# Kernel optimization log

Hardware: AMD Instinct MI355X
Metric: run time of the kernel (lower is better)

Reference implementation:

```python
import math
import jax, jax.numpy as jnp
import numpy as np

N_NODES = 10000
N_EDGES = 160000
N_BASIS = 10
MAX_RADIUS = 5.0
NUM_NEIGHBORS = 16.0
LMAX = 2
MUL_IN = 8
MULS = (32, 16, 10)  # mul[l] = max(4, 32 // (l+1))

# ---------- real Clebsch-Gordan (Wigner) coupling tensors ----------

def _cg_complex(j1, m1, j2, m2, j3, m3):
    if m1 + m2 != m3:
        return 0.0
    f = math.factorial
    pref = math.sqrt((2 * j3 + 1) * f(j1 + j2 - j3) * f(j1 - j2 + j3) * f(-j1 + j2 + j3) / f(j1 + j2 + j3 + 1))
    pref *= math.sqrt(f(j1 + m1) * f(j1 - m1) * f(j2 + m2) * f(j2 - m2) * f(j3 + m3) * f(j3 - m3))
    s = 0.0
    for k in range(max(0, j2 - j3 - m1, j1 - j3 + m2), min(j1 + j2 - j3, j1 - m1, j2 + m2) + 1):
        s += (-1.0) ** k / (f(k) * f(j1 + j2 - j3 - k) * f(j1 - m1 - k) * f(j2 + m2 - k) * f(j3 - j2 + m1 + k) * f(j3 - j1 - m2 + k))
    return pref * s

def _q_matrix(l):
    # complex -> real spherical-harmonic change of basis, rows/cols ordered m = -l..l
    Q = np.zeros((2 * l + 1, 2 * l + 1), dtype=np.complex128)
    Q[l, l] = 1.0
    s2 = 1.0 / math.sqrt(2.0)
    for m in range(1, l + 1):
        Q[l + m, l + m] = (-1) ** m * s2
        Q[l + m, l - m] = s2
        Q[l - m, l - m] = 1j * s2
        Q[l - m, l + m] = -1j * (-1) ** m * s2
    return Q

def _real_cg(l1, l2, l3):
    C = np.zeros((2 * l1 + 1, 2 * l2 + 1, 2 * l3 + 1), dtype=np.complex128)
    for m1 in range(-l1, l1 + 1):
        for m2 in range(-l2, l2 + 1):
            m3 = m1 + m2
            if abs(m3) <= l3:
                C[l1 + m1, l2 + m2, l3 + m3] = _cg_complex(l1, m1, l2, m2, l3, m3)
    K = np.einsum('ia,jb,kc,abc->ijk', _q_matrix(l1).conj(), _q_matrix(l2).conj(), _q_matrix(l3), C)
    K = (1j * K).real if np.abs(K.imag).max() > np.abs(K.real).max() else K.real
    K = K / np.linalg.norm(K) * math.sqrt(2 * l3 + 1)  # component-style path normalization
    return K.astype(np.float32)

PATHS_IN = [(0, 0, 0), (0, 1, 1), (0, 2, 2)]
PATHS_HID = [(li, lf, lo) for li in range(LMAX + 1) for lf in range(LMAX + 1)
             for lo in range(LMAX + 1) if abs(li - lf) <= lo <= li + lf]
PATHS_OUT = [(0, 0, 0), (1, 1, 0), (2, 2, 0)]
CG = {(l1, l2, l3): jnp.asarray(_real_cg(l1, l2, l3))
      for l1 in range(LMAX + 1) for l2 in range(LMAX + 1) for l3 in range(LMAX + 1)
      if abs(l1 - l2) <= l3 <= l1 + l2}

# ---------- edge features ----------

def spherical_harmonics(vec):
    # component-normalized real SH l=0..2 of the normalized edge vector, m = -l..l
    n = vec / jnp.linalg.norm(vec, axis=-1, keepdims=True)
    x, y, z = n[:, 0], n[:, 1], n[:, 2]
    c3, c15, c5 = math.sqrt(3.0), math.sqrt(15.0), math.sqrt(5.0)
    y0 = jnp.ones_like(x)[:, None]
    y1 = c3 * jnp.stack([y, z, x], -1)
    y2 = jnp.stack([c15 * x * y, c15 * y * z, 0.5 * c5 * (3.0 * z * z - 1.0),
                    c15 * x * z, 0.5 * c15 * (x * x - y * y)], -1)
    return {0: y0, 1: y1, 2: y2}

def radial_embedding(r):
    # soft_one_hot_linspace(..., basis='smooth_finite', cutoff=True) * sqrt(n_basis)
    centers = jnp.linspace(0.0, MAX_RADIUS, N_BASIS + 2)[1:-1]
    step = MAX_RADIUS / (N_BASIS + 1)
    d = (r[:, None] - centers) / step
    u = lambda t: jnp.where(t > 0.0, jnp.exp(-1.0 / jnp.where(t > 0.0, t, 1.0)), 0.0)
    return (1.14136 * math.e ** 2 * math.sqrt(N_BASIS)) * u(d + 1.0) * u(1.0 - d)

# ---------- equivariant convolution (gather -> CG tensor product -> scatter) ----------

def conv(feats, edge_src, edge_dst, Y, emb, fw1, fw2, paths, lin):
    n_nodes = feats[0].shape[0]
    w = jax.nn.silu(emb @ fw1) @ fw2            # [E, sum of mul_in over paths]
    by_lo = {0: [], 1: [], 2: []}
    off = 0
    for li, lf, lo in paths:
        f = feats[li][edge_src]                  # gather  [E, mul, 2li+1]
        mul = f.shape[1]
        pw = w[:, off:off + mul]                 # per-edge 'uvu' path weights
        off += mul
        msg = jnp.einsum('eui,ej,ijk,eu->euk', f, Y[lf], CG[(li, lf, lo)], pw)
        by_lo[lo].append(jax.ops.segment_sum(msg, edge_dst, num_segments=n_nodes))
    out = {}
    inv = 1.0 / math.sqrt(NUM_NEIGHBORS)
    for lo, parts in by_lo.items():
        if parts:
            out[lo] = jnp.einsum('nui,uv->nvi', jnp.concatenate(parts, axis=1) * inv, lin[lo])
    return out

def gate(feats, gw):
    s = feats[0][:, :, 0]
    g = jax.nn.sigmoid(s @ gw)                   # [N, mul1 + mul2] gate scalars
    m1 = feats[1].shape[1]
    return {0: jax.nn.silu(feats[0]),
            1: feats[1] * g[:, :m1, None],
            2: feats[2] * g[:, m1:, None]}

# ---------- inputs ----------

def setup_inputs() -> dict:
    ks = iter(jax.random.split(jax.random.key(0), 32))
    def init(shape, fan_in):
        return jax.random.normal(next(ks), shape, jnp.float32) / math.sqrt(fan_in)
    m0, m1, m2 = MULS
    return {
        'x': jax.random.normal(next(ks), (N_NODES, MUL_IN), jnp.float32),
        'edge_vec': 1.2 * jax.random.normal(next(ks), (N_EDGES, 3), jnp.float32),
        'fc1_w1': init((N_BASIS, 100), N_BASIS), 'fc1_w2': init((100, 3 * MUL_IN), 100),
        'lin1_l0': init((MUL_IN, m0), MUL_IN), 'lin1_l1': init((MUL_IN, m1), MUL_IN),
        'lin1_l2': init((MUL_IN, m2), MUL_IN), 'sc1_l0': init((MUL_IN, m0), MUL_IN),
        'gate1_w': init((m0, m1 + m2), m0),
        'fc2_w1': init((N_BASIS, 100), N_BASIS), 'fc2_w2': init((100, 3 * m0 + 6 * m1 + 6 * m2), 100),
        'lin2_l0': init((m0 + m1 + m2, m0), m0 + m1 + m2),
        'lin2_l1': init((m0 + 3 * m1 + 2 * m2, m1), m0 + 3 * m1 + 2 * m2),
        'lin2_l2': init((m0 + 2 * m1 + 3 * m2, m2), m0 + 2 * m1 + 3 * m2),
        'sc2_l0': init((m0, m0), m0), 'sc2_l1': init((m1, m1), m1), 'sc2_l2': init((m2, m2), m2),
        'gate2_w': init((m0, m1 + m2), m0),
        'fc3_w1': init((N_BASIS, 100), N_BASIS), 'fc3_w2': init((100, m0 + m1 + m2), 100),
        'lin3_l0': init((m0 + m1 + m2, 1), m0 + m1 + m2), 'sc3_l0': init((m0, 1), m0),
        'edge_src': jax.random.randint(next(ks), (N_EDGES,), 0, N_NODES),
        'edge_dst': jax.random.randint(next(ks), (N_EDGES,), 0, N_NODES),
    }

def reference(x, edge_vec, fc1_w1, fc1_w2, lin1_l0, lin1_l1, lin1_l2, sc1_l0, gate1_w,
              fc2_w1, fc2_w2, lin2_l0, lin2_l1, lin2_l2, sc2_l0, sc2_l1, sc2_l2, gate2_w,
              fc3_w1, fc3_w2, lin3_l0, sc3_l0, edge_src, edge_dst):
    Y = spherical_harmonics(edge_vec)
    emb = radial_embedding(jnp.linalg.norm(edge_vec, axis=-1))
    # layer 1: 8x0e -> hidden irreps
    h = conv({0: x[:, :, None]}, edge_src, edge_dst, Y, emb, fc1_w1, fc1_w2, PATHS_IN,
             {0: lin1_l0, 1: lin1_l1, 2: lin1_l2})
    h[0] = h[0] + (x @ sc1_l0)[:, :, None]      # self connection (node_attr = 1 -> linear)
    h = gate(h, gate1_w)
    # layer 2: hidden -> hidden, all 15 CG paths
    h2 = conv(h, edge_src, edge_dst, Y, emb, fc2_w1, fc2_w2, PATHS_HID,
              {0: lin2_l0, 1: lin2_l1, 2: lin2_l2})
    h2[0] = h2[0] + jnp.einsum('nui,uv->nvi', h[0], sc2_l0)
    h2[1] = h2[1] + jnp.einsum('nui,uv->nvi', h[1], sc2_l1)
    h2[2] = h2[2] + jnp.einsum('nui,uv->nvi', h[2], sc2_l2)
    h2 = gate(h2, gate2_w)
    # output layer: hidden -> 1x0e
    o = conv(h2, edge_src, edge_dst, Y, emb, fc3_w1, fc3_w2, PATHS_OUT, {0: lin3_l0})
    out = o[0] + jnp.einsum('nui,uv->nvi', h2[0], sc3_l0)
    return out[:, :, 0]                          # [N, 1]
```

## Files before the change

### kernel.cpp

```cpp
#include <hip/hip_runtime.h>
#include <hip/hip_bf16.h>

#define N_NODES 10000
#define N_EDGES 160000

static __device__ const int CG_COMBOS[15][4] = {
  {0,0,0,0},{0,1,1,1},{0,2,2,10},{1,0,1,35},{1,1,0,44},{1,1,1,53},{1,1,2,80},
  {1,2,1,125},{1,2,2,170},{2,0,2,245},{2,1,1,270},{2,1,2,315},{2,2,0,390},
  {2,2,1,415},{2,2,2,490}
};

__device__ inline double factd(int n){ double f=1.0; for(int i=2;i<=n;i++) f*=(double)i; return f; }

__device__ double cg_complex_dev(int j1,int m1,int j2,int m2,int j3,int m3){
  if (m1+m2 != m3) return 0.0;
  double pref = sqrt((2.0*j3+1.0)*factd(j1+j2-j3)*factd(j1-j2+j3)*factd(-j1+j2+j3)/factd(j1+j2+j3+1));
  pref *= sqrt(factd(j1+m1)*factd(j1-m1)*factd(j2+m2)*factd(j2-m2)*factd(j3+m3)*factd(j3-m3));
  int kmin = 0; if (j2-j3-m1 > kmin) kmin = j2-j3-m1; if (j1-j3+m2 > kmin) kmin = j1-j3+m2;
  int kmax = j1+j2-j3; if (j1-m1 < kmax) kmax = j1-m1; if (j2+m2 < kmax) kmax = j2+m2;
  double s = 0.0;
  for (int k=kmin; k<=kmax; ++k){
    double d = factd(k)*factd(j1+j2-j3-k)*factd(j1-m1-k)*factd(j2+m2-k)*factd(j3-j2+m1+k)*factd(j3-j1-m2+k);
    s += ((k&1) ? -1.0 : 1.0)/d;
  }
// ... 86 lines not shown
  __shared__ int lds[1024];
  __shared__ int run_s;
  int tid = threadIdx.x;
  if (tid==0) run_s = 0;
  __syncthreads();
  for (int base=0; base<N_NODES; base+=1024){
    int i = base + tid;
    int vv = (i<N_NODES) ? deg[i] : 0;
    lds[tid]=vv; __syncthreads();
    for (int off=1; off<1024; off<<=1){
      int a = lds[tid];
      int b = (tid>=off) ? lds[tid-off] : 0;
      __syncthreads();
      lds[tid] = a + b;
      __syncthreads();
    }
    int incl = lds[tid];
    int run = run_s;
    if (i < N_NODES){ int ex = run + incl - vv; offs[i]=ex; cursor[i]=ex; }
    __syncthreads();
    if (tid==1023) run_s = run + lds[1023];
    __syncthreads();
  }
  if (tid==0) offs[N_NODES] = run_s;
}

__global__ void scatter_kernel(const int* __restrict__ dst, int* __restrict__ cursor,
                               int* __restrict__ eids, int* __restrict__ pos){
  int e = blockIdx.x*256 + threadIdx.x;
  int p = atomicAdd(&cursor[dst[e]], 1);
  eids[p] = e;
  pos[e] = p;
}

__global__ void perm_kernel(const int* __restrict__ eids, const int* __restrict__ edge_src,
                            const float* __restrict__ edge_vec,
                            int* __restrict__ src_perm, float* __restrict__ vec_perm){
  int p = blockIdx.x*256 + threadIdx.x;
  int e = eids[p];
  src_perm[p] = edge_src[e];
  vec_perm[3*p]   = edge_vec[3*e];
  vec_perm[3*p+1] = edge_vec[3*e+1];
  vec_perm[3*p+2] = edge_vec[3*e+2];
}

template<int WOUT, int WST>
__global__ __launch_bounds__(256) void mlp_kernel(const float* __restrict__ edge_vec,
    const float* __restrict__ w1, const float* __restrict__ w2,
    const int* __restrict__ pos, float* __restrict__ pw){
  __shared__ __align__(16) float emb_s[64*10];
  __shared__ __align__(16) float hid_s[100*64];
  __shared__ int pos_s[64];
  int t = threadIdx.x;
  int eb = blockIdx.x*64;
  if (t < 64){
    int e = eb + t;
    pos_s[t] = pos[e];
    float vx = edge_vec[3*e], vy = edge_vec[3*e+1], vz = edge_vec[3*e+2];
    float r = sqrtf(vx*vx + vy*vy + vz*vz);
    const float EMBC = 1.14136f * 7.3890560989306495f * 3.1622776601683795f;
    #pragma unroll
    for (int bb=0; bb<10; bb++){
      float c = 5.0f*(float)(bb+1)/11.0f;
      float d = (r - c) * (11.0f/5.0f);
      float t1 = d + 1.0f, t2 = 1.0f - d;
      float u1 = (t1 > 0.0f) ? __expf(-1.0f/t1) : 0.0f;
      float u2 = (t2 > 0.0f) ? __expf(-1.0f/t2) : 0.0f;
      emb_s[t*10+bb] = EMBC*u1*u2;
    }
  }
  __syncthreads();
  {
    int e = t & 63, h0 = t >> 6;
    int col = ((e&3)<<4) | (e>>2);
    #pragma unroll
    for (int k=0;k<25;k++){
      int h = h0 + 4*k;
      float s = 0.f;
      #pragma unroll
      for (int bb=0;bb<10;bb++) s += emb_s[e*10+bb]*w1[bb*100+h];
      hid_s[h*64+col] = s/(1.0f+__expf(-s));
    }
  }
  __syncthreads();
  constexpr int NQ = (WOUT+63)/64;
  int cq = t & 63, eg = t >> 6;
  float acc[NQ][16];
  #pragma unroll
  for (int q=0;q<NQ;q++)
    #pragma unroll
    for (int m=0;m<16;m++) acc[q][m]=0.f;
  for (int h=0; h<100; h++){
    float wv[NQ];
    #pragma unroll
    for (int q=0;q<NQ;q++){ int c = cq + 64*q; wv[q] = (c<WOUT) ? w2[h*WOUT+c] : 0.f; }
    const float4* hp = (const float4*)&hid_s[h*64 + (eg<<4)];
    float4 ha = hp[0], hb = hp[1], hc = hp[2], hd = hp[3];
    float hv[16] = {ha.x,ha.y,ha.z,ha.w, hb.x,hb.y,hb.z,hb.w,
                    hc.x,hc.y,hc.z,hc.w, hd.x,hd.y,hd.z,hd.w};
    #pragma unroll
    for (int m=0;m<16;m++){
      #pragma unroll
      for (int q=0;q<NQ;q++) acc[q][m] += wv[q]*hv[m];
    }
  }
  #pragma unroll
  for (int m=0;m<16;m++){
    int row = pos_s[eg + 4*m];
    #pragma unroll
    for (int q=0;q<NQ;q++){
      int c = cq + 64*q;
      if (c < WOUT) pw[(size_t)row*WST + c] = acc[q][m];
    }
  }
}

#define WAVE_SYNC() asm volatile("s_waitcnt lgkmcnt(0)" ::: "memory")

static __device__ const short GP1[3][8] = {
  {0,4,1,1,1,1,0,0},{4,4,4,1,3,3,1,1},{8,8,8,1,5,5,4,10}
};
static __device__ const short GP3[3][8] = {
  {0,8,1,1,1,1,0,0},{8,8,1,3,1,3,1,44},{16,8,1,5,1,5,4,390}
};
static __device__ const short GP2[15][8] = {
  {0,4,1,1,1,1,0,0},
  {4,4,4,1,3,3,1,1},
  {8,8,8,1,5,5,4,10},
  {16,12,4,3,3,1,0,35},
  {28,4,1,3,1,3,1,44},
  {32,12,4,3,3,3,1,53},
  {44,24,8,3,5,3,1,80},
  {68,12,4,3,3,5,4,125},
  {80,24,8,3,5,5,4,170},
  {104,40,8,5,5,1,0,245},
  {144,20,4,5,3,3,1,270},
  {164,40,8,5,5,3,1,315},
  {204,8,1,5,1,5,4,390},
  {212,20,4,5,3,5,4,415},
  {232,40,8,5,5,5,4,490}
};

static __device__ const short L2RS[9][3][5] = {
  {{0,32,  0,0,  0},{0,0,0,0,0},{0,0,0,0,0}},
  {{0,32, 32,0,  4},{0,0,0,0,0},{0,0,0,0,0}},
  {{0,32, 64,0,  8},{0,0,0,0,0},{0,0,0,0,0}},
  {{0,16,112,1, 28},{0,0,0,0,0},{0,0,0,0,0}},
  {{0,16, 96,1, 16},{16,32,128,1,32},{32,48,160,1,68}},
  {{0,16,144,1, 44},{16,32,176,1,80},{0,0,0,0,0}},
  {{0,10,222,2,204},{0,0,0,0,0},{0,0,0,0,0}},
  {{0,10,202,2,144},{10,20,232,2,212},{0,0,0,0,0}},
  {{0,10,192,2,104},{10,20,212,2,164},{20,30,242,2,232}}
};
static __device__ const short L2CB[9][3] = {
  {0,0,0},{58,0,0},{358,0,0},{32,0,0},{154,202,250},{518,598,0},{48,0,0},{298,328,0},{678,728,778}
};

template<int NI,int NK>
__device__ inline void mac_seg(const float* __restrict__ fS, const float* __restrict__ gS,
                               const float* __restrict__ pS, unsigned d, float* a){
  float p = pS[d & 255];
  int fb = (d>>8)&255, gb = (int)(d>>16);
  float f[5];
  if constexpr (NI==1){ f[0]=fS[fb]*p; }
  else if constexpr (NI==3){
    float4 t=*(const float4*)(fS+fb); f[0]=t.x*p; f[1]=t.y*p; f[2]=t.z*p;
  } else {
    float4 t=*(const float4*)(fS+fb); f[0]=t.x*p;f[1]=t.y*p;f[2]=t.z*p;f[3]=t.w*p; f[4]=fS[fb+4]*p;
  }
  if constexpr (NK==1){
    if constexpr (NI==1){ a[0] += f[0]*gS[gb]; }
    else {
      float4 g=*(const float4*)(gS+gb);
      float s = f[0]*g.x + f[1]*g.y + f[2]*g.z;
      if constexpr (NI==5) s += f[3]*g.w + f[4]*gS[gb+4];
      a[0] += s;
    }
  } else {
    constexpr int ST = (NK==3)?4:8;
    #pragma unroll
    for (int i=0;i<NI;i++){
      float4 g=*(const float4*)(gS+gb+i*ST);
      a[0]+=f[i]*g.x; a[1]+=f[i]*g.y; a[2]+=f[i]*g.z;
      if constexpr (NK==5){ a[3]+=f[i]*g.w; a[4]+=f[i]*gS[gb+i*ST+4]; }
    }
  }
}

__device__ inline void mac_seg_l3(const float* __restrict__ fS, const float* __restrict__ gS,
                                  const float* __restrict__ pS, unsigned d, float* a){
  float p = pS[d & 255];
  int fb = (d>>8)&255, gb = (int)(d>>16);
  float4 g=*(const float4*)(gS+gb); float g4=gS[gb+4];
  float s = fS[fb]*g.x + fS[fb+1]*g.y + fS[fb+2]*g.z + fS[fb+3]*g.w + fS[fb+4]*g4;
  a[0] += p*s;
}

template<int LAYER>
__global__ __launch_bounds__(64,3) void conv_kernel(
    const int* __restrict__ offs,
    const int* __restrict__ src_perm, const float* __restrict__ vec_perm,
    const float* __restrict__ cgbuf, const float* __restrict__ pw,
    const float* __restrict__ fin,
    const float* __restrict__ linA, const float* __restrict__ linB, const float* __restrict__ linC,
    const float* __restrict__ scA, const float* __restrict__ scB, const float* __restrict__ scC,
    const float* __restrict__ gw,
    float* __restrict__ outp)
{
  constexpr int C     = (LAYER==1) ? 72  : (LAYER==2) ? 828 : 58;
  constexpr int WST   = (LAYER==1) ? 24  : (LAYER==2) ? 252 : 60;
  constexpr int PWSZ  = (LAYER==1) ? 24  : (LAYER==2) ? 252 : 60;
  constexpr int PWL4  = (LAYER==1) ? 6   : (LAYER==2) ? 63  : 15;
  constexpr int FLDS  = (LAYER==1) ? 8   : 180;
  constexpr int GTOTP = (LAYER==1) ? 16  : (LAYER==2) ? 272 : 24;
  constexpr int GR    = (LAYER==2) ? 5 : 1;
  constexpr int NP    = (LAYER==2) ? 15 : 3;
  constexpr int NACC  = (LAYER==1) ? 5 : (LAYER==2) ? 27 : 1;

  __shared__ __align__(16) float pw_s[PWSZ];
  __shared__ __align__(16) float f_s[FLDS];
  __shared__ __align__(16) float G_s[GTOTP];
  __shared__ __align__(16) float row_s[C];
  __shared__ __align__(16) float s0_s[32];
  __shared__ __align__(16) float g_s[26];

  const int lane = threadIdx.x;
  const int n = blockIdx.x;

  int rm[3] = {-1,-1,-1};
  if constexpr (LAYER != 1){
    #pragma unroll
    for (int r=0;r<3;r++){
      int i = lane + 64*r;
      if (i < 32) rm[r] = i;
      else if (i < 80)  rm[r] = 32 + ((i-32)/3)*4 + (i-32)%3;
      else if (i < 130) rm[r] = 96 + ((i-80)/5)*8 + (i-80)%5;
    }
  }

  unsigned md[9]; int cbs[9]; int l1nk = 0;
  #pragma unroll
  for (int r=0;r<9;r++){ md[r]=0; cbs[r]=0; }
  if constexpr (LAYER==2){
    constexpr int RNKc[9] = {1,3,5,1,3,5,1,3,5};
    #pragma unroll
    for (int r=0;r<9;r++){
      #pragma unroll
      for (int s=0;s<3;s++){
        int lo = L2RS[r][s][0], hi = L2RS[r][s][1];
        if (hi > lo && lane >= lo && lane < hi){
          int u = lane - lo;
          int fc = L2RS[r][s][3];
          int flds = (fc==0) ? u : (fc==1) ? 32+4*u : 96+8*u;
          md[r] = (unsigned)(L2RS[r][s][2]+u) | ((unsigned)flds<<8) | ((unsigned)L2RS[r][s][4]<<16);
          cbs[r] = L2CB[r][s] + u*RNKc[r];
        }
      }
    }
  } else if constexpr (LAYER==1){
    if (lane < 24){
      int grp = lane >> 3, u = lane & 7;
      int gb = (grp==0) ? 0 : (grp==1) ? 4 : 8;
      md[0] = (unsigned)(grp*8+u) | ((unsigned)u<<8) | ((unsigned)gb<<16);
      cbs[0] = (grp==0) ? u : (grp==1) ? 8+3*u : 32+5*u;
      l1nk = (grp==0) ? 1 : (grp==1) ? 3 : 5;
    }
  } else {
    if (lane < 58){
      int grp = (lane<32) ? 0 : (lane<48) ? 1 : 2;
      int u = lane - ((grp==0)?0:(grp==1)?32:48);
      int flds = (grp==0) ? u : (grp==1) ? 32+4*u : 96+8*u;
      int gb = (grp==0) ? 0 : (grp==1) ? 8 : 16;
      md[0] = (unsigned)(((grp==0)?0:(grp==1)?32:48)+u) | ((unsigned)flds<<8) | ((unsigned)gb<<16);
      cbs[0] = (grp==0) ? u : (grp==1) ? 32+u : 48+u;
    }
  }

  float cgr[GR][5];
  bool gc0[GR], gc1[GR];
  #pragma unroll
  for (int rg=0;rg<GR;rg++){
    #pragma unroll
    for (int j=0;j<5;j++) cgr[rg][j] = 0.f;
    gc0[rg] = true; gc1[rg] = false;
    int g = lane + 64*rg;
    if (g < GTOTP){
      for (int p=0;p<NP;p++){
        const short* P = (LAYER==1) ? GP1[p] : (LAYER==2) ? GP2[p] : GP3[p];
        int base = P[0], alloc = P[1];
        if (g >= base && g < base+alloc){
          int S = P[2], ni = P[3], nk = P[4], nj = P[5], yb = P[6], cgo = P[7];
          int i, k; bool valid;
          if (S == 1){ i = g - base; k = 0; valid = (i < ni); }
          else { i = (g-base)/S; k = (g-base)%S; valid = (k < nk); }
          gc0[rg] = (yb == 0); gc1[rg] = (yb == 1);
          if (valid){
            #pragma unroll
            for (int j=0;j<5;j++)
              if (j < nj) cgr[rg][j] = cgbuf[cgo + (i*nj+j)*nk + k];
          } else {
            gc0[rg] = true;
          }
        }
      }
    }
  }

  float acc[NACC];
  #pragma unroll
  for (int i=0;i<NACC;i++) acc[i] = 0.f;

  int beg = offs[n], end = offs[n+1];

  for (int idx=beg; idx<end; ++idx){
    int src = src_perm[idx];
    float vx = vec_perm[3*idx], vy = vec_perm[3*idx+1], vz = vec_perm[3*idx+2];

    float4 pwv = {0,0,0,0};
    if (lane < PWL4) pwv = *(const float4*)&pw[(size_t)idx*WST + lane*4];
    float fv[3] = {0,0,0};
    if constexpr (LAYER==1){
      if (lane < 8) fv[0] = fin[(size_t)src*8 + lane];
    } else {
      #pragma unroll
      for (int r=0;r<3;r++){
        int i = lane + 64*r;
        if (i < 130) fv[r] = fin[(size_t)src*130 + i];
      }
    }

    float rinv = rsqrtf(vx*vx + vy*vy + vz*vz);
    float X = vx*rinv, Yv = vy*rinv, Z = vz*rinv;
    const float c3 = 1.7320508075688772f, c15 = 3.872983346207417f;
    float y1 = c3*Yv, y2 = c3*Z, y3 = c3*X;
    float y4 = c15*X*Yv, y5 = c15*Yv*Z, y6 = 1.118033988749895f*(3.f*Z*Z-1.f);
    float y7 = c15*X*Z, y8 = 0.5f*c15*(X*X - Yv*Yv);

    WAVE_SYNC();

    if (lane < PWL4) *(float4*)&pw_s[lane*4] = pwv;
    if constexpr (LAYER==1){
      if (lane < 8) f_s[lane] = fv[0];
    } else {
      #pragma unroll
      for (int r=0;r<3;r++) if (rm[r] >= 0) f_s[rm[r]] = fv[r];
    }

    #pragma unroll
    for (int rg=0;rg<GR;rg++){
      int g = lane + 64*rg;
      if (g < GTOTP){
        float ya = gc1[rg] ? y1 : y4;
        float yb2 = gc1[rg] ? y2 : y5;
        float yc = gc1[rg] ? y3 : y6;
        float t = cgr[rg][0]*ya + cgr[rg][1]*yb2 + cgr[rg][2]*yc + cgr[rg][3]*y7 + cgr[rg][4]*y8;
        G_s[g] = gc0[rg] ? cgr[rg][0] : t;
      }
    }

    WAVE_SYNC();

    if constexpr (LAYER==2){
      if (lane<32) mac_seg<1,1>(f_s,G_s,pw_s,md[0],&acc[0]);
      if (lane<32) mac_seg<1,3>(f_s,G_s,pw_s,md[1],&acc[1]);
      if (lane<32) mac_seg<1,5>(f_s,G_s,pw_s,md[2],&acc[4]);
      if (lane<16) mac_seg<3,1>(f_s,G_s,pw_s,md[3],&acc[9]);
      if (lane<48) mac_seg<3,3>(f_s,G_s,pw_s,md[4],&acc[10]);
      if (lane<32) mac_seg<3,5>(f_s,G_s,pw_s,md[5],&acc[13]);
      if (lane<10) mac_seg<5,1>(f_s,G_s,pw_s,md[6],&acc[18]);
      if (lane<20) mac_seg<5,3>(f_s,G_s,pw_s,md[7],&acc[19]);
      if (lane<30) mac_seg<5,5>(f_s,G_s,pw_s,md[8],&acc[22]);
    } else if constexpr (LAYER==1){
      if (lane<24) mac_seg<1,5>(f_s,G_s,pw_s,md[0],&acc[0]);
    } else {
      if (lane<58) mac_seg_l3(f_s,G_s,pw_s,md[0],&acc[0]);
    }
  }

  WAVE_SYNC();
  constexpr float inv = 0.25f;
  if constexpr (LAYER==2){
    constexpr int RNKc[9] = {1,3,5,1,3,5,1,3,5};
    constexpr int AB[9]   = {0,1,4,9,10,13,18,19,22};
    constexpr int CNTc[9] = {32,32,32,16,48,32,10,20,30};
    #pragma unroll
    for (int r=0;r<9;r++){
      if (lane < CNTc[r]){
        #pragma unroll
        for (int k=0;k<RNKc[r];k++) row_s[cbs[r]+k] = acc[AB[r]+k]*inv;
      }
    }
  } else if constexpr (LAYER==1){
    if (lane < 24){
      #pragma unroll
      for (int k=0;k<5;k++) if (k < l1nk) row_s[cbs[0]+k] = acc[k]*inv;
    }
  } else {
    if (lane < 58) row_s[cbs[0]] = acc[0]*inv;
  }

  if constexpr (LAYER==1){
    if (lane < 8) f_s[lane] = fin[(size_t)n*8 + lane];
  } else {
    #pragma unroll
    for (int r=0;r<3;r++){
      int i = lane + 64*r;
      if (i < 130 && rm[r] >= 0) f_s[rm[r]] = fin[(size_t)n*130 + i];
    }
  }
  WAVE_SYNC();

  if constexpr (LAYER==3){
    float v = 0.f;
    if (lane < 58) v += row_s[lane]*linA[lane];
    if (lane < 32) v += f_s[lane]*scA[lane];
    #pragma unroll
    for (int d=32; d>0; d>>=1) v += __shfl_down(v, d, 64);
    if (lane==0) outp[n] = v;
  } else {
    constexpr int NU0  = (LAYER==1) ? 8 : 58;
    constexpr int NSC0 = (LAYER==1) ? 8 : 32;
    if (lane < 32){
      float s = 0.f;
      for (int u=0;u<NU0;u++)  s += row_s[u]*linA[u*32+lane];
      for (int u=0;u<NSC0;u++) s += f_s[u]*scA[u*32+lane];
      s0_s[lane] = s;
    }
    WAVE_SYNC();
    if (lane < 26){
      float s = 0.f;
      for (int v2=0;v2<32;v2++) s += s0_s[v2]*gw[v2*26+lane];
      g_s[lane] = 1.f/(1.f + __expf(-s));
    }
    WAVE_SYNC();
    for (int c=lane;c<130;c+=64){
      float val;
      if (c < 32){
        float s = s0_s[c];
        val = s/(1.f + __expf(-s));
      } else if (c < 80){
        int u = (c-32)/3, k = (c-32)%3;
        float s = 0.f;
        if constexpr (LAYER==1){
          for (int up=0;up<8;up++) s += row_s[8 + up*3 + k]*linB[up*16+u];
        } else {
          for (int U=0;U<100;U++)  s += row_s[58 + U*3 + k]*linB[U*16+u];
          for (int up=0;up<16;up++) s += f_s[32 + up*4 + k]*scB[up*16+u];
        }
        val = s*g_s[u];
      } else {
        int u = (c-80)/5, k = (c-80)%5;
        float s = 0.f;
        if constexpr (LAYER==1){
          for (int up=0;up<8;up++) s += row_s[32 + up*5 + k]*linC[up*10+u];
        } else {
          for (int U=0;U<94;U++)   s += row_s[358 + U*5 + k]*linC[U*10+u];
          for (int up=0;up<10;up++) s += f_s[96 + up*8 + k]*scC[up*10+u];
        }
        val = s*g_s[16+u];
      }
      outp[(size_t)n*130 + c] = val;
    }
  }
}

extern "C" void kernel_launch(void* const* d_in, const int* in_sizes, int n_in,
                              void* d_out, int out_size, void* d_ws, size_t ws_size,
                              hipStream_t stream){
  (void)in_sizes; (void)n_in; (void)out_size; (void)ws_size;
  const float* x        = (const float*)d_in[0];
  const float* edge_vec = (const float*)d_in[1];
  const float* fc1_w1   = (const float*)d_in[2];
  const float* fc1_w2   = (const float*)d_in[3];
  const float* lin1_l0  = (const float*)d_in[4];
  const float* lin1_l1  = (const float*)d_in[5];
  const float* lin1_l2  = (const float*)d_in[6];
  const float* sc1_l0   = (const float*)d_in[7];
  const float* gate1_w  = (const float*)d_in[8];
  const float* fc2_w1   = (const float*)d_in[9];
  const float* fc2_w2   = (const float*)d_in[10];
  const float* lin2_l0  = (const float*)d_in[11];
  const float* lin2_l1  = (const float*)d_in[12];
  const float* lin2_l2  = (const float*)d_in[13];
  const float* sc2_l0   = (const float*)d_in[14];
  const float* sc2_l1   = (const float*)d_in[15];
  const float* sc2_l2   = (const float*)d_in[16];
  const float* gate2_w  = (const float*)d_in[17];
  const float* fc3_w1   = (const float*)d_in[18];
  const float* fc3_w2   = (const float*)d_in[19];
  const float* lin3_l0  = (const float*)d_in[20];
  const float* sc3_l0   = (const float*)d_in[21];
  const int* edge_src   = (const int*)d_in[22];
  const int* edge_dst   = (const int*)d_in[23];
  float* out = (float*)d_out;

  char* base = (char*)d_ws;
  size_t off = 0;
  auto carve = [&](size_t bytes)->char*{
    char* p = base + off;
    off = (off + bytes + 255) & ~(size_t)255;
    return p;
  };
  int*   deg      = (int*)  carve((size_t)N_NODES*4);
  int*   offs     = (int*)  carve((size_t)(N_NODES+1)*4);
  int*   cursor   = (int*)  carve((size_t)N_NODES*4);
  int*   eids     = (int*)  carve((size_t)N_EDGES*4);
  int*   pos      = (int*)  carve((size_t)N_EDGES*4);
  int*   src_perm = (int*)  carve((size_t)N_EDGES*4);
  float* vec_perm = (float*)carve((size_t)N_EDGES*12);
  float* cgbuf    = (float*)carve(615*4);
  float* hfeats   = (float*)carve((size_t)N_NODES*130*4);
  float* h2feats  = (float*)carve((size_t)N_NODES*130*4);
  float* pwbuf    = (float*)carve((size_t)N_EDGES*252*4);

  hipMemsetAsync(deg, 0, (size_t)N_NODES*4, stream);
  hist_kernel<<<N_EDGES/256, 256, 0, stream>>>(edge_dst, deg);
  scan_kernel<<<1, 1024, 0, stream>>>(deg, offs, cursor);
  scatter_kernel<<<N_EDGES/256, 256, 0, stream>>>(edge_dst, cursor, eids, pos);
  perm_kernel<<<N_EDGES/256, 256, 0, stream>>>(eids, edge_src, edge_vec, src_perm, vec_perm);
  cg_init_kernel<<<15, 128, 0, stream>>>(cgbuf);

  mlp_kernel<24,24><<<N_EDGES/64, 256, 0, stream>>>(edge_vec, fc1_w1, fc1_w2, pos, pwbuf);
  conv_kernel<1><<<N_NODES, 64, 0, stream>>>(offs, src_perm, vec_perm, cgbuf, pwbuf,
      x, lin1_l0, lin1_l1, lin1_l2, sc1_l0, nullptr, nullptr, gate1_w, hfeats);
  mlp_kernel<252,252><<<N_EDGES/64, 256, 0, stream>>>(edge_vec, fc2_w1, fc2_w2, pos, pwbuf);
  conv_kernel<2><<<N_NODES, 64, 0, stream>>>(offs, src_perm, vec_perm, cgbuf, pwbuf,
      hfeats, lin2_l0, lin2_l1, lin2_l2, sc2_l0, sc2_l1, sc2_l2, gate2_w, h2feats);
  mlp_kernel<58,60><<<N_EDGES/64, 256, 0, stream>>>(edge_vec, fc3_w1, fc3_w2, pos, pwbuf);
  conv_kernel<3><<<N_NODES, 64, 0, stream>>>(offs, src_perm, vec_perm, cgbuf, pwbuf,
      h2feats, lin3_l0, nullptr, nullptr, sc3_l0, nullptr, nullptr, nullptr, out);
}
```

Baseline: 652.8 us.

## Load per-edge features and weights straight to registers; transpose accumulator layout

```diff
diff --git a/kernel.cpp b/kernel.cpp
--- a/kernel.cpp
+++ b/kernel.cpp
@@ -262,22 +262,16 @@
   {{0,10,202,2,144},{10,20,232,2,212},{0,0,0,0,0}},
   {{0,10,192,2,104},{10,20,212,2,164},{20,30,242,2,232}}
 };
-static __device__ const short L2CB[9][3] = {
-  {0,0,0},{58,0,0},{358,0,0},{32,0,0},{154,202,250},{518,598,0},{48,0,0},{298,328,0},{678,728,778}
+static __device__ const short L2CBN[9][3] = {
+  {0,0,0},{60,0,0},{360,0,0},{32,0,0},{92,108,124},{392,408,0},{48,0,0},{140,150,0},{424,434,444}
 };
 
 template<int NI,int NK>
-__device__ inline void mac_seg(const float* __restrict__ fS, const float* __restrict__ gS,
-                               const float* __restrict__ pS, unsigned d, float* a){
-  float p = pS[d & 255];
-  int fb = (d>>8)&255, gb = (int)(d>>16);
+__device__ inline void mac2(const float* fv, float p, int gb,
+                            const float* __restrict__ gS, float* a){
   float f[5];
-  if constexpr (NI==1){ f[0]=fS[fb]*p; }
-  else if constexpr (NI==3){
-    float4 t=*(const float4*)(fS+fb); f[0]=t.x*p; f[1]=t.y*p; f[2]=t.z*p;
-  } else {
-    float4 t=*(const float4*)(fS+fb); f[0]=t.x*p;f[1]=t.y*p;f[2]=t.z*p;f[3]=t.w*p; f[4]=fS[fb+4]*p;
-  }
+  #pragma unroll
+  for (int i=0;i<NI;i++) f[i] = fv[i]*p;
   if constexpr (NK==1){
     if constexpr (NI==1){ a[0] += f[0]*gS[gb]; }
     else {
@@ -297,17 +291,8 @@
   }
 }
 
-__device__ inline void mac_seg_l3(const float* __restrict__ fS, const float* __restrict__ gS,
-                                  const float* __restrict__ pS, unsigned d, float* a){
-  float p = pS[d & 255];
-  int fb = (d>>8)&255, gb = (int)(d>>16);
-  float4 g=*(const float4*)(gS+gb); float g4=gS[gb+4];
-  float s = fS[fb]*g.x + fS[fb+1]*g.y + fS[fb+2]*g.z + fS[fb+3]*g.w + fS[fb+4]*g4;
-  a[0] += p*s;
-}
-
 template<int LAYER>
-__global__ __launch_bounds__(64,3) void conv_kernel(
+__global__ __launch_bounds__(64) void conv_kernel(
     const int* __restrict__ offs,
     const int* __restrict__ src_perm, const float* __restrict__ vec_perm,
     const float* __restrict__ cgbuf, const float* __restrict__ pw,
@@ -317,18 +302,14 @@
     const float* __restrict__ gw,
     float* __restrict__ outp)
 {
-  constexpr int C     = (LAYER==1) ? 72  : (LAYER==2) ? 828 : 58;
+  constexpr int C     = (LAYER==1) ? 72  : (LAYER==2) ? 840 : 58;
   constexpr int WST   = (LAYER==1) ? 24  : (LAYER==2) ? 252 : 60;
-  constexpr int PWSZ  = (LAYER==1) ? 24  : (LAYER==2) ? 252 : 60;
-  constexpr int PWL4  = (LAYER==1) ? 6   : (LAYER==2) ? 63  : 15;
-  constexpr int FLDS  = (LAYER==1) ? 8   : 180;
+  constexpr int FIN   = (LAYER==1) ? 8   : 130;
   constexpr int GTOTP = (LAYER==1) ? 16  : (LAYER==2) ? 272 : 24;
   constexpr int GR    = (LAYER==2) ? 5 : 1;
   constexpr int NP    = (LAYER==2) ? 15 : 3;
   constexpr int NACC  = (LAYER==1) ? 5 : (LAYER==2) ? 27 : 1;
 
-  __shared__ __align__(16) float pw_s[PWSZ];
-  __shared__ __align__(16) float f_s[FLDS];
   __shared__ __align__(16) float G_s[GTOTP];
   __shared__ __align__(16) float row_s[C];
   __shared__ __align__(16) float s0_s[32];
@@ -337,22 +318,10 @@
   const int lane = threadIdx.x;
   const int n = blockIdx.x;
 
-  int rm[3] = {-1,-1,-1};
-  if constexpr (LAYER != 1){
-    #pragma unroll
-    for (int r=0;r<3;r++){
-      int i = lane + 64*r;
-      if (i < 32) rm[r] = i;
-      else if (i < 80)  rm[r] = 32 + ((i-32)/3)*4 + (i-32)%3;
-      else if (i < 130) rm[r] = 96 + ((i-80)/5)*8 + (i-80)%5;
-    }
-  }
-
   unsigned md[9]; int cbs[9]; int l1nk = 0;
   #pragma unroll
   for (int r=0;r<9;r++){ md[r]=0; cbs[r]=0; }
   if constexpr (LAYER==2){
-    constexpr int RNKc[9] = {1,3,5,1,3,5,1,3,5};
     #pragma unroll
     for (int r=0;r<9;r++){
       #pragma unroll
@@ -361,9 +330,9 @@
         if (hi > lo && lane >= lo && lane < hi){
           int u = lane - lo;
           int fc = L2RS[r][s][3];
-          int flds = (fc==0) ? u : (fc==1) ? 32+4*u : 96+8*u;
-          md[r] = (unsigned)(L2RS[r][s][2]+u) | ((unsigned)flds<<8) | ((unsigned)L2RS[r][s][4]<<16);
-          cbs[r] = L2CB[r][s] + u*RNKc[r];
+          int fo = (fc==0) ? u : (fc==1) ? 32+3*u : 80+5*u;
+          md[r] = (unsigned)(L2RS[r][s][2]+u) | ((unsigned)fo<<8) | ((unsigned)L2RS[r][s][4]<<16);
+          cbs[r] = L2CBN[r][s] + u;
         }
       }
     }
@@ -372,16 +341,16 @@
       int grp = lane >> 3, u = lane & 7;
       int gb = (grp==0) ? 0 : (grp==1) ? 4 : 8;
       md[0] = (unsigned)(grp*8+u) | ((unsigned)u<<8) | ((unsigned)gb<<16);
-      cbs[0] = (grp==0) ? u : (grp==1) ? 8+3*u : 32+5*u;
+      cbs[0] = (grp==0) ? u : (grp==1) ? 8+u : 32+u;
       l1nk = (grp==0) ? 1 : (grp==1) ? 3 : 5;
     }
   } else {
     if (lane < 58){
       int grp = (lane<32) ? 0 : (lane<48) ? 1 : 2;
       int u = lane - ((grp==0)?0:(grp==1)?32:48);
-      int flds = (grp==0) ? u : (grp==1) ? 32+4*u : 96+8*u;
+      int fo = (grp==0) ? u : (grp==1) ? 32+3*u : 80+5*u;
       int gb = (grp==0) ? 0 : (grp==1) ? 8 : 16;
-      md[0] = (unsigned)(((grp==0)?0:(grp==1)?32:48)+u) | ((unsigned)flds<<8) | ((unsigned)gb<<16);
+      md[0] = (unsigned)(((grp==0)?0:(grp==1)?32:48)+u) | ((unsigned)fo<<8) | ((unsigned)gb<<16);
       cbs[0] = (grp==0) ? u : (grp==1) ? 32+u : 48+u;
     }
   }
@@ -420,23 +389,45 @@
   #pragma unroll
   for (int i=0;i<NACC;i++) acc[i] = 0.f;
 
-  int beg = offs[n], end = offs[n+1];
+  int beg = __builtin_amdgcn_readfirstlane(offs[n]);
+  int end = __builtin_amdgcn_readfirstlane(offs[n+1]);
 
   for (int idx=beg; idx<end; ++idx){
-    int src = src_perm[idx];
+    int src = __builtin_amdgcn_readfirstlane(src_perm[idx]);
+    const float* frow  = fin + (size_t)src*FIN;
+    const float* pwrow = pw  + (size_t)idx*WST;
     float vx = vec_perm[3*idx], vy = vec_perm[3*idx+1], vz = vec_perm[3*idx+2];
 
-    float4 pwv = {0,0,0,0};
-    if (lane < PWL4) pwv = *(const float4*)&pw[(size_t)idx*WST + lane*4];
-    float fv[3] = {0,0,0};
-    if constexpr (LAYER==1){
-      if (lane < 8) fv[0] = fin[(size_t)src*8 + lane];
+    float pv[9], f1v[3], f3v[3][3], f5v[3][5];
+    if constexpr (LAYER==2){
+      if (lane < 32){
+        #pragma unroll
+        for (int r=0;r<3;r++){ pv[r]=pwrow[md[r]&255]; f1v[r]=frow[(md[r]>>8)&255]; }
+      }
+      if (lane < 16){ pv[3]=pwrow[md[3]&255]; int fb=(md[3]>>8)&255;
+        #pragma unroll
+        for (int i=0;i<3;i++) f3v[0][i]=frow[fb+i]; }
+      if (lane < 48){ pv[4]=pwrow[md[4]&255]; int fb=(md[4]>>8)&255;
+        #pragma unroll
+        for (int i=0;i<3;i++) f3v[1][i]=frow[fb+i]; }
+      if (lane < 32){ pv[5]=pwrow[md[5]&255]; int fb=(md[5]>>8)&255;
+        #pragma unroll
+        for (int i=0;i<3;i++) f3v[2][i]=frow[fb+i]; }
+      if (lane < 10){ pv[6]=pwrow[md[6]&255]; int fb=(md[6]>>8)&255;
+        #pragma unroll
+        for (int i=0;i<5;i++) f5v[0][i]=frow[fb+i]; }
+      if (lane < 20){ pv[7]=pwrow[md[7]&255]; int fb=(md[7]>>8)&255;
+        #pragma unroll
+        for (int i=0;i<5;i++) f5v[1][i]=frow[fb+i]; }
+      if (lane < 30){ pv[8]=pwrow[md[8]&255]; int fb=(md[8]>>8)&255;
+        #pragma unroll
+        for (int i=0;i<5;i++) f5v[2][i]=frow[fb+i]; }
+    } else if constexpr (LAYER==1){
+      if (lane < 24){ pv[0]=pwrow[md[0]&255]; f1v[0]=frow[(md[0]>>8)&255]; }
     } else {
-      #pragma unroll
-      for (int r=0;r<3;r++){
-        int i = lane + 64*r;
-        if (i < 130) fv[r] = fin[(size_t)src*130 + i];
-      }
+      if (lane < 58){ pv[0]=pwrow[md[0]&255]; int fb=(md[0]>>8)&255;
+        #pragma unroll
+        for (int i=0;i<5;i++) f5v[0][i]=frow[fb+i]; }
     }
 
     float rinv = rsqrtf(vx*vx + vy*vy + vz*vz);
@@ -448,21 +439,13 @@
 
     WAVE_SYNC();
 
-    if (lane < PWL4) *(float4*)&pw_s[lane*4] = pwv;
-    if constexpr (LAYER==1){
-      if (lane < 8) f_s[lane] = fv[0];
-    } else {
-      #pragma unroll
-      for (int r=0;r<3;r++) if (rm[r] >= 0) f_s[rm[r]] = fv[r];
-    }
-
     #pragma unroll
     for (int rg=0;rg<GR;rg++){
       int g = lane + 64*rg;
       if (g < GTOTP){
-        float ya = gc1[rg] ? y1 : y4;
+        float ya  = gc1[rg] ? y1 : y4;
         float yb2 = gc1[rg] ? y2 : y5;
-        float yc = gc1[rg] ? y3 : y6;
+        float yc  = gc1[rg] ? y3 : y6;
         float t = cgr[rg][0]*ya + cgr[rg][1]*yb2 + cgr[rg][2]*yc + cgr[rg][3]*y7 + cgr[rg][4]*y8;
         G_s[g] = gc0[rg] ? cgr[rg][0] : t;
       }
@@ -471,19 +454,21 @@
     WAVE_SYNC();
 
     if constexpr (LAYER==2){
-      if (lane<32) mac_seg<1,1>(f_s,G_s,pw_s,md[0],&acc[0]);
-      if (lane<32) mac_seg<1,3>(f_s,G_s,pw_s,md[1],&acc[1]);
-      if (lane<32) mac_seg<1,5>(f_s,G_s,pw_s,md[2],&acc[4]);
-      if (lane<16) mac_seg<3,1>(f_s,G_s,pw_s,md[3],&acc[9]);
-      if (lane<48) mac_seg<3,3>(f_s,G_s,pw_s,md[4],&acc[10]);
-      if (lane<32) mac_seg<3,5>(f_s,G_s,pw_s,md[5],&acc[13]);
-      if (lane<10) mac_seg<5,1>(f_s,G_s,pw_s,md[6],&acc[18]);
-      if (lane<20) mac_seg<5,3>(f_s,G_s,pw_s,md[7],&acc[19]);
-      if (lane<30) mac_seg<5,5>(f_s,G_s,pw_s,md[8],&acc[22]);
+      if (lane<32){
+        mac2<1,1>(&f1v[0], pv[0], (int)(md[0]>>16), G_s, &acc[0]);
+        mac2<1,3>(&f1v[1], pv[1], (int)(md[1]>>16), G_s, &acc[1]);
+        mac2<1,5>(&f1v[2], pv[2], (int)(md[2]>>16), G_s, &acc[4]);
+      }
+      if (lane<16) mac2<3,1>(f3v[0], pv[3], (int)(md[3]>>16), G_s, &acc[9]);
+      if (lane<48) mac2<3,3>(f3v[1], pv[4], (int)(md[4]>>16), G_s, &acc[10]);
+      if (lane<32) mac2<3,5>(f3v[2], pv[5], (int)(md[5]>>16), G_s, &acc[13]);
+      if (lane<10) mac2<5,1>(f5v[0], pv[6], (int)(md[6]>>16), G_s, &acc[18]);
+      if (lane<20) mac2<5,3>(f5v[1], pv[7], (int)(md[7]>>16), G_s, &acc[19]);
+      if (lane<30) mac2<5,5>(f5v[2], pv[8], (int)(md[8]>>16), G_s, &acc[22]);
     } else if constexpr (LAYER==1){
-      if (lane<24) mac_seg<1,5>(f_s,G_s,pw_s,md[0],&acc[0]);
+      if (lane<24) mac2<1,5>(&f1v[0], pv[0], (int)(md[0]>>16), G_s, &acc[0]);
     } else {
-      if (lane<58) mac_seg_l3(f_s,G_s,pw_s,md[0],&acc[0]);
+      if (lane<58) mac2<5,1>(f5v[0], pv[0], (int)(md[0]>>16), G_s, &acc[0]);
     }
   }
 
@@ -493,37 +478,30 @@
     constexpr int RNKc[9] = {1,3,5,1,3,5,1,3,5};
     constexpr int AB[9]   = {0,1,4,9,10,13,18,19,22};
     constexpr int CNTc[9] = {32,32,32,16,48,32,10,20,30};
+    constexpr int KSc[9]  = {0,100,96,0,100,96,0,100,96};
     #pragma unroll
     for (int r=0;r<9;r++){
       if (lane < CNTc[r]){
         #pragma unroll
-        for (int k=0;k<RNKc[r];k++) row_s[cbs[r]+k] = acc[AB[r]+k]*inv;
+        for (int k=0;k<RNKc[r];k++) row_s[cbs[r]+k*KSc[r]] = acc[AB[r]+k]*inv;
       }
     }
   } else if constexpr (LAYER==1){
     if (lane < 24){
       #pragma unroll
-      for (int k=0;k<5;k++) if (k < l1nk) row_s[cbs[0]+k] = acc[k]*inv;
+      for (int k=0;k<5;k++) if (k < l1nk) row_s[cbs[0]+k*8] = acc[k]*inv;
     }
   } else {
     if (lane < 58) row_s[cbs[0]] = acc[0]*inv;
   }
-
-  if constexpr (LAYER==1){
-    if (lane < 8) f_s[lane] = fin[(size_t)n*8 + lane];
-  } else {
-    #pragma unroll
-    for (int r=0;r<3;r++){
-      int i = lane + 64*r;
-      if (i < 130 && rm[r] >= 0) f_s[rm[r]] = fin[(size_t)n*130 + i];
-    }
-  }
   WAVE_SYNC();
+
+  const float* fo = fin + (size_t)n*FIN;
 
   if constexpr (LAYER==3){
     float v = 0.f;
     if (lane < 58) v += row_s[lane]*linA[lane];
-    if (lane < 32) v += f_s[lane]*scA[lane];
+    if (lane < 32) v += fo[lane]*scA[lane];
     #pragma unroll
     for (int d=32; d>0; d>>=1) v += __shfl_down(v, d, 64);
     if (lane==0) outp[n] = v;
@@ -533,7 +511,7 @@
     if (lane < 32){
       float s = 0.f;
       for (int u=0;u<NU0;u++)  s += row_s[u]*linA[u*32+lane];
-      for (int u=0;u<NSC0;u++) s += f_s[u]*scA[u*32+lane];
+      for (int u=0;u<NSC0;u++) s += fo[u]*scA[u*32+lane];
       s0_s[lane] = s;
     }
     WAVE_SYNC();
@@ -552,20 +530,39 @@
         int u = (c-32)/3, k = (c-32)%3;
         float s = 0.f;
         if constexpr (LAYER==1){
-          for (int up=0;up<8;up++) s += row_s[8 + up*3 + k]*linB[up*16+u];
+          const float4* rp = (const float4*)&row_s[8+k*8];
+          float4 r0 = rp[0], r1 = rp[1];
+          s = r0.x*linB[0*16+u]+r0.y*linB[1*16+u]+r0.z*linB[2*16+u]+r0.w*linB[3*16+u]
+            + r1.x*linB[4*16+u]+r1.y*linB[5*16+u]+r1.z*linB[6*16+u]+r1.w*linB[7*16+u];
         } else {
-          for (int U=0;U<100;U++)  s += row_s[58 + U*3 + k]*linB[U*16+u];
-          for (int up=0;up<16;up++) s += f_s[32 + up*4 + k]*scB[up*16+u];
+          const float4* rp = (const float4*)&row_s[60+k*100];
+          #pragma unroll 5
+          for (int q=0;q<25;q++){
+            float4 rv = rp[q];
+            s += rv.x*linB[(4*q+0)*16+u] + rv.y*linB[(4*q+1)*16+u]
+               + rv.z*linB[(4*q+2)*16+u] + rv.w*linB[(4*q+3)*16+u];
+          }
+          for (int up=0;up<16;up++) s += fo[32+up*3+k]*scB[up*16+u];
         }
         val = s*g_s[u];
       } else {
         int u = (c-80)/5, k = (c-80)%5;
         float s = 0.f;
         if constexpr (LAYER==1){
-          for (int up=0;up<8;up++) s += row_s[32 + up*5 + k]*linC[up*10+u];
+          const float4* rp = (const float4*)&row_s[32+k*8];
+          float4 r0 = rp[0], r1 = rp[1];
+          s = r0.x*linC[0*10+u]+r0.y*linC[1*10+u]+r0.z*linC[2*10+u]+r0.w*linC[3*10+u]
+            + r1.x*linC[4*10+u]+r1.y*linC[5*10+u]+r1.z*linC[6*10+u]+r1.w*linC[7*10+u];
         } else {
-          for (int U=0;U<94;U++)   s += row_s[358 + U*5 + k]*linC[U*10+u];
-          for (int up=0;up<10;up++) s += f_s[96 + up*8 + k]*scC[up*10+u];
+          const float4* rp = (const float4*)&row_s[360+k*96];
+          #pragma unroll 5
+          for (int q=0;q<23;q++){
+            float4 rv = rp[q];
+            s += rv.x*linC[(4*q+0)*10+u] + rv.y*linC[(4*q+1)*10+u]
+               + rv.z*linC[(4*q+2)*10+u] + rv.w*linC[(4*q+3)*10+u];
+          }
+          s += row_s[360+k*96+92]*linC[92*10+u] + row_s[360+k*96+93]*linC[93*10+u];
+          for (int up=0;up<10;up++) s += fo[80+up*5+k]*scC[up*10+u];
         }
         val = s*g_s[16+u];
       }
```

Measured after the change: 772.7 us. 18.4% more time.

## Pack four node-waves per block and transpose row buffer for vectorized epilogue

Applied to the files above, without the earlier changes.

```diff
diff --git a/kernel.cpp b/kernel.cpp
--- a/kernel.cpp
+++ b/kernel.cpp
@@ -262,8 +262,8 @@
   {{0,10,202,2,144},{10,20,232,2,212},{0,0,0,0,0}},
   {{0,10,192,2,104},{10,20,212,2,164},{20,30,242,2,232}}
 };
-static __device__ const short L2CB[9][3] = {
-  {0,0,0},{58,0,0},{358,0,0},{32,0,0},{154,202,250},{518,598,0},{48,0,0},{298,328,0},{678,728,778}
+static __device__ const short L2CBN[9][3] = {
+  {0,0,0},{60,0,0},{360,0,0},{32,0,0},{92,108,124},{392,408,0},{48,0,0},{140,150,0},{424,434,444}
 };
 
 template<int NI,int NK>
@@ -307,7 +307,7 @@
 }
 
 template<int LAYER>
-__global__ __launch_bounds__(64,3) void conv_kernel(
+__global__ __launch_bounds__(256,6) void conv_kernel(
     const int* __restrict__ offs,
     const int* __restrict__ src_perm, const float* __restrict__ vec_perm,
     const float* __restrict__ cgbuf, const float* __restrict__ pw,
@@ -317,25 +317,34 @@
     const float* __restrict__ gw,
     float* __restrict__ outp)
 {
-  constexpr int C     = (LAYER==1) ? 72  : (LAYER==2) ? 828 : 58;
   constexpr int WST   = (LAYER==1) ? 24  : (LAYER==2) ? 252 : 60;
-  constexpr int PWSZ  = (LAYER==1) ? 24  : (LAYER==2) ? 252 : 60;
-  constexpr int PWL4  = (LAYER==1) ? 6   : (LAYER==2) ? 63  : 15;
-  constexpr int FLDS  = (LAYER==1) ? 8   : 180;
+  constexpr int PWL4  = WST/4;
+  constexpr int FIN   = (LAYER==1) ? 8   : 130;
   constexpr int GTOTP = (LAYER==1) ? 16  : (LAYER==2) ? 272 : 24;
   constexpr int GR    = (LAYER==2) ? 5 : 1;
   constexpr int NP    = (LAYER==2) ? 15 : 3;
   constexpr int NACC  = (LAYER==1) ? 5 : (LAYER==2) ? 27 : 1;
-
-  __shared__ __align__(16) float pw_s[PWSZ];
-  __shared__ __align__(16) float f_s[FLDS];
-  __shared__ __align__(16) float G_s[GTOTP];
-  __shared__ __align__(16) float row_s[C];
-  __shared__ __align__(16) float s0_s[32];
-  __shared__ __align__(16) float g_s[26];
-
-  const int lane = threadIdx.x;
-  const int n = blockIdx.x;
+  constexpr int PWPAD = (LAYER==1) ? 32 : (LAYER==2) ? 256 : 64;
+  constexpr int FPAD  = (LAYER==1) ? 16 : 180;
+  constexpr int GOFF  = PWPAD + FPAD;
+  constexpr int ROWSZ = (LAYER==1) ? 72 : (LAYER==2) ? 840 : 58;
+  constexpr int LOOPSZ= GOFF + GTOTP;
+  constexpr int EPISZ = (LAYER==3) ? 58 : ROWSZ + 64;
+  constexpr int RMAX  = (LOOPSZ > EPISZ) ? LOOPSZ : EPISZ;
+  constexpr int R     = ((RMAX + 15)/16)*16;
+
+  __shared__ __align__(16) float smem[4*R];
+
+  const int lane = threadIdx.x & 63;
+  const int wav  = threadIdx.x >> 6;
+  const int n    = blockIdx.x*4 + wav;
+
+  float* __restrict__ pw_s = smem + wav*R;
+  float* __restrict__ f_s  = pw_s + PWPAD;
+  float* __restrict__ G_s  = pw_s + GOFF;
+  float* __restrict__ row_s= pw_s;
+  float* __restrict__ s0_s = pw_s + ROWSZ;
+  float* __restrict__ g_s  = pw_s + ROWSZ + 32;
 
   int rm[3] = {-1,-1,-1};
   if constexpr (LAYER != 1){
@@ -352,7 +361,6 @@
   #pragma unroll
   for (int r=0;r<9;r++){ md[r]=0; cbs[r]=0; }
   if constexpr (LAYER==2){
-    constexpr int RNKc[9] = {1,3,5,1,3,5,1,3,5};
     #pragma unroll
     for (int r=0;r<9;r++){
       #pragma unroll
@@ -363,7 +371,7 @@
           int fc = L2RS[r][s][3];
           int flds = (fc==0) ? u : (fc==1) ? 32+4*u : 96+8*u;
           md[r] = (unsigned)(L2RS[r][s][2]+u) | ((unsigned)flds<<8) | ((unsigned)L2RS[r][s][4]<<16);
-          cbs[r] = L2CB[r][s] + u*RNKc[r];
+          cbs[r] = L2CBN[r][s] + u;
         }
       }
     }
@@ -372,7 +380,7 @@
       int grp = lane >> 3, u = lane & 7;
       int gb = (grp==0) ? 0 : (grp==1) ? 4 : 8;
       md[0] = (unsigned)(grp*8+u) | ((unsigned)u<<8) | ((unsigned)gb<<16);
-      cbs[0] = (grp==0) ? u : (grp==1) ? 8+3*u : 32+5*u;
+      cbs[0] = (grp==0) ? u : (grp==1) ? 8+u : 32+u;
       l1nk = (grp==0) ? 1 : (grp==1) ? 3 : 5;
     }
   } else {
@@ -460,9 +468,9 @@
     for (int rg=0;rg<GR;rg++){
       int g = lane + 64*rg;
       if (g < GTOTP){
-        float ya = gc1[rg] ? y1 : y4;
+        float ya  = gc1[rg] ? y1 : y4;
         float yb2 = gc1[rg] ? y2 : y5;
-        float yc = gc1[rg] ? y3 : y6;
+        float yc  = gc1[rg] ? y3 : y6;
         float t = cgr[rg][0]*ya + cgr[rg][1]*yb2 + cgr[rg][2]*yc + cgr[rg][3]*y7 + cgr[rg][4]*y8;
         G_s[g] = gc0[rg] ? cgr[rg][0] : t;
       }
@@ -471,9 +479,11 @@
     WAVE_SYNC();
 
     if constexpr (LAYER==2){
-      if (lane<32) mac_seg<1,1>(f_s,G_s,pw_s,md[0],&acc[0]);
-      if (lane<32) mac_seg<1,3>(f_s,G_s,pw_s,md[1],&acc[1]);
-      if (lane<32) mac_seg<1,5>(f_s,G_s,pw_s,md[2],&acc[4]);
+      if (lane<32){
+        mac_seg<1,1>(f_s,G_s,pw_s,md[0],&acc[0]);
+        mac_seg<1,3>(f_s,G_s,pw_s,md[1],&acc[1]);
+        mac_seg<1,5>(f_s,G_s,pw_s,md[2],&acc[4]);
+      }
       if (lane<16) mac_seg<3,1>(f_s,G_s,pw_s,md[3],&acc[9]);
       if (lane<48) mac_seg<3,3>(f_s,G_s,pw_s,md[4],&acc[10]);
       if (lane<32) mac_seg<3,5>(f_s,G_s,pw_s,md[5],&acc[13]);
@@ -493,37 +503,30 @@
     constexpr int RNKc[9] = {1,3,5,1,3,5,1,3,5};
     constexpr int AB[9]   = {0,1,4,9,10,13,18,19,22};
     constexpr int CNTc[9] = {32,32,32,16,48,32,10,20,30};
+    constexpr int KSc[9]  = {0,100,96,0,100,96,0,100,96};
     #pragma unroll
     for (int r=0;r<9;r++){
       if (lane < CNTc[r]){
         #pragma unroll
-        for (int k=0;k<RNKc[r];k++) row_s[cbs[r]+k] = acc[AB[r]+k]*inv;
+        for (int k=0;k<RNKc[r];k++) row_s[cbs[r]+k*KSc[r]] = acc[AB[r]+k]*inv;
       }
     }
   } else if constexpr (LAYER==1){
     if (lane < 24){
       #pragma unroll
-      for (int k=0;k<5;k++) if (k < l1nk) row_s[cbs[0]+k] = acc[k]*inv;
+      for (int k=0;k<5;k++) if (k < l1nk) row_s[cbs[0]+k*8] = acc[k]*inv;
     }
   } else {
     if (lane < 58) row_s[cbs[0]] = acc[0]*inv;
   }
-
-  if constexpr (LAYER==1){
-    if (lane < 8) f_s[lane] = fin[(size_t)n*8 + lane];
-  } else {
-    #pragma unroll
-    for (int r=0;r<3;r++){
-      int i = lane + 64*r;
-      if (i < 130 && rm[r] >= 0) f_s[rm[r]] = fin[(size_t)n*130 + i];
-    }
-  }
   WAVE_SYNC();
+
+  const float* fo = fin + (size_t)n*FIN;
 
   if constexpr (LAYER==3){
     float v = 0.f;
     if (lane < 58) v += row_s[lane]*linA[lane];
-    if (lane < 32) v += f_s[lane]*scA[lane];
+    if (lane < 32) v += fo[lane]*scA[lane];
     #pragma unroll
     for (int d=32; d>0; d>>=1) v += __shfl_down(v, d, 64);
     if (lane==0) outp[n] = v;
@@ -533,7 +536,7 @@
     if (lane < 32){
       float s = 0.f;
       for (int u=0;u<NU0;u++)  s += row_s[u]*linA[u*32+lane];
-      for (int u=0;u<NSC0;u++) s += f_s[u]*scA[u*32+lane];
+      for (int u=0;u<NSC0;u++) s += fo[u]*scA[u*32+lane];
       s0_s[lane] = s;
     }
     WAVE_SYNC();
@@ -552,20 +555,39 @@
         int u = (c-32)/3, k = (c-32)%3;
         float s = 0.f;
         if constexpr (LAYER==1){
-          for (int up=0;up<8;up++) s += row_s[8 + up*3 + k]*linB[up*16+u];
+          const float4* rp = (const float4*)&row_s[8+k*8];
+          float4 r0 = rp[0], r1 = rp[1];
+          s = r0.x*linB[0*16+u]+r0.y*linB[1*16+u]+r0.z*linB[2*16+u]+r0.w*linB[3*16+u]
+            + r1.x*linB[4*16+u]+r1.y*linB[5*16+u]+r1.z*linB[6*16+u]+r1.w*linB[7*16+u];
         } else {
-          for (int U=0;U<100;U++)  s += row_s[58 + U*3 + k]*linB[U*16+u];
-          for (int up=0;up<16;up++) s += f_s[32 + up*4 + k]*scB[up*16+u];
+          const float4* rp = (const float4*)&row_s[60+k*100];
+          #pragma unroll 5
+          for (int q=0;q<25;q++){
+            float4 rv = rp[q];
+            s += rv.x*linB[(4*q+0)*16+u] + rv.y*linB[(4*q+1)*16+u]
+               + rv.z*linB[(4*q+2)*16+u] + rv.w*linB[(4*q+3)*16+u];
+          }
+          for (int up=0;up<16;up++) s += fo[32+up*3+k]*scB[up*16+u];
         }
         val = s*g_s[u];
       } else {
         int u = (c-80)/5, k = (c-80)%5;
         float s = 0.f;
         if constexpr (LAYER==1){
-          for (int up=0;up<8;up++) s += row_s[32 + up*5 + k]*linC[up*10+u];
+          const float4* rp = (const float4*)&row_s[32+k*8];
+          float4 r0 = rp[0], r1 = rp[1];
+          s = r0.x*linC[0*10+u]+r0.y*linC[1*10+u]+r0.z*linC[2*10+u]+r0.w*linC[3*10+u]
+            + r1.x*linC[4*10+u]+r1.y*linC[5*10+u]+r1.z*linC[6*10+u]+r1.w*linC[7*10+u];
         } else {
-          for (int U=0;U<94;U++)   s += row_s[358 + U*5 + k]*linC[U*10+u];
-          for (int up=0;up<10;up++) s += f_s[96 + up*8 + k]*scC[up*10+u];
+          const float4* rp = (const float4*)&row_s[360+k*96];
+          #pragma unroll 5
+          for (int q=0;q<23;q++){
+            float4 rv = rp[q];
+            s += rv.x*linC[(4*q+0)*10+u] + rv.y*linC[(4*q+1)*10+u]
+               + rv.z*linC[(4*q+2)*10+u] + rv.w*linC[(4*q+3)*10+u];
+          }
+          s += row_s[360+k*96+92]*linC[92*10+u] + row_s[360+k*96+93]*linC[93*10+u];
+          for (int up=0;up<10;up++) s += fo[80+up*5+k]*scC[up*10+u];
         }
         val = s*g_s[16+u];
       }
@@ -631,12 +653,12 @@
   cg_init_kernel<<<15, 128, 0, stream>>>(cgbuf);
 
   mlp_kernel<24,24><<<N_EDGES/64, 256, 0, stream>>>(edge_vec, fc1_w1, fc1_w2, pos, pwbuf);
-  conv_kernel<1><<<N_NODES, 64, 0, stream>>>(offs, src_perm, vec_perm, cgbuf, pwbuf,
+  conv_kernel<1><<<(N_NODES+3)/4, 256, 0, stream>>>(offs, src_perm, vec_perm, cgbuf, pwbuf,
       x, lin1_l0, lin1_l1, lin1_l2, sc1_l0, nullptr, nullptr, gate1_w, hfeats);
   mlp_kernel<252,252><<<N_EDGES/64, 256, 0, stream>>>(edge_vec, fc2_w1, fc2_w2, pos, pwbuf);
-  conv_kernel<2><<<N_NODES, 64, 0, stream>>>(offs, src_perm, vec_perm, cgbuf, pwbuf,
+  conv_kernel<2><<<(N_NODES+3)/4, 256, 0, stream>>>(offs, src_perm, vec_perm, cgbuf, pwbuf,
       hfeats, lin2_l0, lin2_l1, lin2_l2, sc2_l0, sc2_l1, sc2_l2, gate2_w, h2feats);
   mlp_kernel<58,60><<<N_EDGES/64, 256, 0, stream>>>(edge_vec, fc3_w1, fc3_w2, pos, pwbuf);
-  conv_kernel<3><<<N_NODES, 64, 0, stream>>>(offs, src_perm, vec_perm, cgbuf, pwbuf,
+  conv_kernel<3><<<(N_NODES+3)/4, 256, 0, stream>>>(offs, src_perm, vec_perm, cgbuf, pwbuf,
       h2feats, lin3_l0, nullptr, nullptr, sc3_l0, nullptr, nullptr, nullptr, out);
 }
```

New measurement: 939.6 us. 1.44x slower.
